# Kernel optimization log

Hardware: AMD Instinct MI355X
Metric: run time of the kernel (lower is better)

Reference implementation:

```python
import jax, jax.numpy as jnp
import numpy as np

N, C, H, W = 64, 128, 32, 32
EPS = 1e-5


def _layernorm_chw(x, w, b):
    # LayerNorm over normalized_shape=(C,H,W): last 3 dims
    mu = jnp.mean(x, axis=(1, 2, 3), keepdims=True)
    var = jnp.var(x, axis=(1, 2, 3), keepdims=True)
    return (x - mu) * jax.lax.rsqrt(var + EPS) * w[None] + b[None]


def _conv1x1(x, w, b):
    # x: [N,C,H,W], w: [Cout,Cin], b: [Cout]
    return jnp.einsum('oc,nchw->nohw', w, x) + b[None, :, None, None]


def setup_inputs() -> dict:
    key = jax.random.key(0)
    ks = jax.random.split(key, 12)
    d = {
        'query': jax.random.normal(ks[0], (N, C, H, W), jnp.float32),
        'key': jax.random.normal(ks[1], (N, C, H, W), jnp.float32),
        'value': jax.random.normal(ks[2], (N, C, H, W), jnp.float32),
        'ln1_w': jnp.ones((C, H, W), jnp.float32),
        'ln1_b': jnp.zeros((C, H, W), jnp.float32),
        'ln2_w': jnp.ones((C, H, W), jnp.float32),
        'ln2_b': jnp.zeros((C, H, W), jnp.float32),
        'ln3_w': jnp.ones((C, H, W), jnp.float32),
        'ln3_b': jnp.zeros((C, H, W), jnp.float32),
        'wq': jax.random.normal(ks[3], (C, C), jnp.float32) / np.sqrt(C),
        'bq': jnp.zeros((C,), jnp.float32),
        'wk': jax.random.normal(ks[4], (C, C), jnp.float32) / np.sqrt(C),
        'bk': jnp.zeros((C,), jnp.float32),
        'wv': jax.random.normal(ks[5], (C, C), jnp.float32) / np.sqrt(C),
        'bv': jnp.zeros((C,), jnp.float32),
    }
    return d


def reference(query, key, value, ln1_w, ln1_b, ln2_w, ln2_b, ln3_w, ln3_b,
              wq, bq, wk, bk, wv, bv):
    qn = _layernorm_chw(query, ln1_w, ln1_b)  # residual uses normalized query
    kn = _layernorm_chw(key, ln2_w, ln2_b)
    vn = _layernorm_chw(value, ln3_w, ln3_b)
    q = _conv1x1(qn, wq, bq).reshape(N, C, H * W)
    k = _conv1x1(kn, wk, bk).reshape(N, C, H * W)
    v = _conv1x1(vn, wv, bv).reshape(N, C, H * W)
    # attention[n,i,j] = sum_c k[n,c,i] q[n,c,j] / sqrt(C); softmax over i (dim=1)
    attn = jnp.einsum('nci,ncj->nij', k, q) / jnp.sqrt(jnp.float32(C))
    attn = jax.nn.softmax(attn, axis=1)
    out = jnp.einsum('nci,nij->ncj', v, attn).reshape(N, C, H, W)
    x = qn + out
    return x.reshape(N, -1)  # flatten(start_dim=1)
```

## Files before the change

kernel.cpp:

```cpp
#include <hip/hip_runtime.h>


#define NS 64
#define CD 128
#define SD 1024
#define MEL (CD*SD)
#define SCALE 0.08838834764831845f

typedef __attribute__((ext_vector_type(4))) float floatx4;
typedef __attribute__((ext_vector_type(8))) short short8;
typedef __attribute__((ext_vector_type(4))) short short4v;

typedef __attribute__((address_space(1))) const void global_cvoid;
typedef __attribute__((address_space(3))) void lds_void;

__device__ __forceinline__ void gl16(const void* g, void* l) {
  __builtin_amdgcn_global_load_lds((global_cvoid*)g, (lds_void*)l, 16, 0, 0);
}
__device__ __forceinline__ unsigned short f2bf(float f) {
  union { float f; unsigned int i; } v; v.f = f;
  unsigned int i = v.i;
  return (unsigned short)((i + 0x7fffu + ((i >> 16) & 1u)) >> 16);
}
__device__ __forceinline__ short8 ld8_bf16(const float* __restrict__ p) {
  floatx4 a = *(const floatx4*)p;
  floatx4 b = *(const floatx4*)(p + 4);
  short8 r;
  r[0] = (short)f2bf(a[0]); r[1] = (short)f2bf(a[1]);
  r[2] = (short)f2bf(a[2]); r[3] = (short)f2bf(a[3]);
  r[4] = (short)f2bf(b[0]); r[5] = (short)f2bf(b[1]);
  r[6] = (short)f2bf(b[2]); r[7] = (short)f2bf(b[3]);
  return r;
}
__device__ __forceinline__ floatx4 mfma16(short8 a, short8 b, floatx4 c) {
  return __builtin_amdgcn_mfma_f32_16x16x32_bf16(a, b, c, 0, 0, 0);
}

__global__ __launch_bounds__(512) void stats_kernel(
    const float* __restrict__ q, const float* __restrict__ k,
    const float* __restrict__ v, float* __restrict__ sums)
{
  int tn = blockIdx.x;
  int part = blockIdx.y;
  int t = tn >> 6;
  const float* x = (t == 0 ? q : (t == 1 ? k : v)) + (size_t)(tn & 63) * MEL
                   + part * (MEL / 2);
  float s1 = 0.f, s2 = 0.f;
  for (int it = 0; it < 32; ++it) {
    floatx4 u = *(const floatx4*)(x + it * 2048 + threadIdx.x * 4);
#pragma unroll
    for (int j = 0; j < 4; ++j) { float f = u[j]; s1 += f; s2 += f * f; }
  }
#pragma unroll
  for (int off = 32; off; off >>= 1) {
    s1 += __shfl_xor(s1, off, 64);
    s2 += __shfl_xor(s2, off, 64);
  }
  __shared__ float r1[8], r2[8];
  int w = threadIdx.x >> 6;
  if ((threadIdx.x & 63) == 0) { r1[w] = s1; r2[w] = s2; }
  __syncthreads();
  if (threadIdx.x == 0) {
    float a = 0.f, b = 0.f;
#pragma unroll
    for (int i = 0; i < 8; ++i) { a += r1[i]; b += r2[i]; }
    sums[part * 192 + tn] = a; sums[384 + part * 192 + tn] = b;
  }
}

__global__ __launch_bounds__(512, 4) void proj_kernel(
  const float* __restrict__ k, const float* __restrict__ v,
  const float* __restrict__ l2w, const float* __restrict__ l2b,
  const float* __restrict__ l3w, const float* __restrict__ l3b,
  const float* __restrict__ wk, const float* __restrict__ bk,
  const float* __restrict__ wv, const float* __restrict__ bv,
  const float* __restrict__ sums,
  unsigned short* __restrict__ kT, unsigned short* __restrict__ vN)
{
  int n  = blockIdx.x, t = blockIdx.y, st = blockIdx.z;
  const float* x  = (t == 0 ? k : v) + (size_t)n * MEL;
  const float* lw = (t == 0 ? l2w : l3w);
  const float* lb = (t == 0 ? l2b : l3b);
  const float* W  = (t == 0 ? wk : wv);
  const float* Bs = (t == 0 ? bk : bv);

  int si = (t + 1) * 64 + n;
  float s1 = sums[si] + sums[192 + si];
  float s2 = sums[384 + si] + sums[576 + si];
  float mu  = s1 * (1.f / MEL);
  float var = s2 * (1.f / MEL) - mu * mu;
  float rs  = rsqrtf(var + 1e-5f);
  float a_ln = rs, b_ln = -mu * rs;

  __shared__ __align__(16) unsigned short Xt[128 * 128];

  int tid = threadIdx.x;
  int cb = tid & 15, sb = (tid >> 4) & 15, half = tid >> 8;
  int s0 = st * 128;

  unsigned int w32[8][2];
#pragma unroll
  for (int pr = 0; pr < 2; ++pr) {
    int c0 = cb * 8 + half * 4 + pr * 2;
    const float* xp0 = x  + (size_t)c0 * SD + s0 + sb * 8;
    const float* wp0 = lw + (size_t)c0 * SD + s0 + sb * 8;
    const float* bp0 = lb + (size_t)c0 * SD + s0 + sb * 8;
    float xv0[8], xv1[8], wv0[8], wv1[8], bv0[8], bv1[8];
    *(floatx4*)xv0 = *(const floatx4*)xp0;       *(floatx4*)(xv0+4) = *(const floatx4*)(xp0+4);
    *(floatx4*)xv1 = *(const floatx4*)(xp0+SD);  *(floatx4*)(xv1+4) = *(const floatx4*)(xp0+SD+4);
    *(floatx4*)wv0 = *(const floatx4*)wp0;       *(floatx4*)(wv0+4) = *(const floatx4*)(wp0+4);
    *(floatx4*)wv1 = *(const floatx4*)(wp0+SD);  *(floatx4*)(wv1+4) = *(const floatx4*)(wp0+SD+4);
    *(floatx4*)bv0 = *(const floatx4*)bp0;       *(floatx4*)(bv0+4) = *(const floatx4*)(bp0+4);
    *(floatx4*)bv1 = *(const floatx4*)(bp0+SD);  *(floatx4*)(bv1+4) = *(const floatx4*)(bp0+SD+4);
#pragma unroll
    for (int js = 0; js < 8; ++js) {
      unsigned int lo = f2bf((xv0[js] * a_ln + b_ln) * wv0[js] + bv0[js]);
      unsigned int hi = f2bf((xv1[js] * a_ln + b_ln) * wv1[js] + bv1[js]);
      w32[js][pr] = lo | (hi << 16);
    }
  }
#pragma unroll
  for (int js = 0; js < 8; ++js) {
    unsigned int* d = (unsigned int*)&Xt[(sb * 8 + js) * 128 + ((cb ^ js) * 8) + half * 4];
    d[0] = w32[js][0]; d[1] = w32[js][1];
  }
  __syncthreads();

  int lane = tid & 63, w = tid >> 6;
  int quad = lane >> 4, l16 = lane & 15;

  short8 Wf[4];
#pragma unroll
  for (int kk = 0; kk < 4; ++kk)
    Wf[kk] = ld8_bf16(W + (w * 16 + l16) * CD + kk * 32 + quad * 8);

  floatx4 acc[8];
  floatx4 zz = {0.f, 0.f, 0.f, 0.f};
#pragma unroll
  for (int sblk = 0; sblk < 8; ++sblk) acc[sblk] = zz;
#pragma unroll
  for (int kk = 0; kk < 4; ++kk)
#pragma unroll
    for (int sblk = 0; sblk < 8; ++sblk) {
      short8 Xf = *(const short8*)&Xt[(sblk * 16 + l16) * 128 +
                                      (((kk * 4 + quad) ^ (l16 & 7)) * 8)];
      acc[sblk] = (t == 0) ? mfma16(Wf[kk], Xf, acc[sblk])
                           : mfma16(Xf, Wf[kk], acc[sblk]);
    }
  __syncthreads();

  if (t == 0) {
    float bsv[4];
#pragma unroll
    for (int r = 0; r < 4; ++r) bsv[r] = Bs[w * 16 + quad * 4 + r];
#pragma unroll
    for (int sblk = 0; sblk < 8; ++sblk) {
      short4v pk;
#pragma unroll
      for (int r = 0; r < 4; ++r) pk[r] = (short)f2bf(acc[sblk][r] + bsv[r]);
      int row = sblk * 16 + l16;
      int cblk = w * 2 + (quad >> 1);
      *(short4v*)&Xt[row * 128 + ((cblk ^ (l16 & 7)) * 8) + (quad & 1) * 4] = pk;
    }
  } else {
    float bsv = Bs[w * 16 + l16];
#pragma unroll
    for (int sblk = 0; sblk < 8; ++sblk) {
      short4v pk;
#pragma unroll
      for (int r = 0; r < 4; ++r) pk[r] = (short)f2bf(acc[sblk][r] + bsv);
      int row = w * 16 + l16;
      int cblk = sblk * 2 + (quad >> 1);
      *(short4v*)&Xt[row * 128 + ((cblk ^ (l16 & 7)) * 8) + (quad & 1) * 4] = pk;
    }
  }
  __syncthreads();

  unsigned short* outp = (t == 0 ? kT : vN);
#pragma unroll
  for (int it = 0; it < 4; ++it) {
    int id = it * 512 + tid;
    int row = id >> 4, ch = id & 15;
    short8 u = *(const short8*)&Xt[row * 128 + ((ch ^ (row & 7)) * 8)];
    size_t g;
    if (t == 0) g = (size_t)n * MEL + (size_t)(s0 + row) * CD + ch * 8;
    else        g = (size_t)n * MEL + (size_t)row * SD + s0 + ch * 8;
    *(short8*)(outp + g) = u;
  }
}

__global__ __launch_bounds__(512, 4) void attn_kernel(
  const float* __restrict__ qraw, const float* __restrict__ l1w,
  const float* __restrict__ l1b, const float* __restrict__ wq,
  const float* __restrict__ bq,
  const unsigned short* __restrict__ kT, const unsigned short* __restrict__ vN,
  const float* __restrict__ sums, float* __restrict__ out)
{
  int n = blockIdx.x, jt = blockIdx.y;
  int j0 = jt * 128;

  __shared__ __align__(16) char smem[33792];
  unsigned short* Xt = (unsigned short*)smem;
  unsigned short* Ks = (unsigned short*)smem;
  unsigned short* Ps = (unsigned short*)smem;
  unsigned short* Vs = (unsigned short*)(smem + 16384);
  float* l_part = (float*)(smem + 32768);

  int tid = threadIdx.x, lane = tid & 63, w = tid >> 6;
  int quad = lane >> 4, l16 = lane & 15;

  float s1 = sums[n] + sums[192 + n];
  float s2 = sums[384 + n] + sums[576 + n];
  float mu  = s1 * (1.f / MEL);
  float var = s2 * (1.f / MEL) - mu * mu;
  float rsd = rsqrtf(var + 1e-5f);
  float a_ln = rsd, b_ln = -mu * rsd;
  const float* qb = qraw + (size_t)n * MEL;

  {
    int cb = tid & 15, sb = (tid >> 4) & 15, half = tid >> 8;
    unsigned int w32[8][2];
#pragma unroll
    for (int pr = 0; pr < 2; ++pr) {
      int c0 = cb * 8 + half * 4 + pr * 2;
      const float* xp0 = qb  + (size_t)c0 * SD + j0 + sb * 8;
      const float* wp0 = l1w + (size_t)c0 * SD + j0 + sb * 8;
      const float* bp0 = l1b + (size_t)c0 * SD + j0 + sb * 8;
      float xv0[8], xv1[8], wv0[8], wv1[8], bv0[8], bv1[8];
      *(floatx4*)xv0 = *(const floatx4*)xp0;       *(floatx4*)(xv0+4) = *(const floatx4*)(xp0+4);
      *(floatx4*)xv1 = *(const floatx4*)(xp0+SD);  *(floatx4*)(xv1+4) = *(const floatx4*)(xp0+SD+4);
      *(floatx4*)wv0 = *(const floatx4*)wp0;       *(floatx4*)(wv0+4) = *(const floatx4*)(wp0+4);
      *(floatx4*)wv1 = *(const floatx4*)(wp0+SD);  *(floatx4*)(wv1+4) = *(const floatx4*)(wp0+SD+4);
      *(floatx4*)bv0 = *(const floatx4*)bp0;       *(floatx4*)(bv0+4) = *(const floatx4*)(bp0+4);
      *(floatx4*)bv1 = *(const floatx4*)(bp0+SD);  *(floatx4*)(bv1+4) = *(const floatx4*)(bp0+SD+4);
#pragma unroll
      for (int js = 0; js < 8; ++js) {
        unsigned int lo = f2bf((xv0[js] * a_ln + b_ln) * wv0[js] + bv0[js]);
        unsigned int hi = f2bf((xv1[js] * a_ln + b_ln) * wv1[js] + bv1[js]);
        w32[js][pr] = lo | (hi << 16);
      }
    }
#pragma unroll
    for (int js = 0; js < 8; ++js) {
      unsigned int* d = (unsigned int*)&Xt[(sb * 8 + js) * 128 + ((cb ^ js) * 8) + half * 4];
      d[0] = w32[js][0]; d[1] = w32[js][1];
    }
  }
  __syncthreads();

  floatx4 zz = {0.f, 0.f, 0.f, 0.f};
  {
    short8 Wf[4];
#pragma unroll
    for (int kk = 0; kk < 4; ++kk)
      Wf[kk] = ld8_bf16(wq + (w * 16 + l16) * CD + kk * 32 + quad * 8);
    floatx4 accq[8];
#pragma unroll
    for (int nb = 0; nb < 8; ++nb) accq[nb] = zz;
#pragma unroll
    for (int kk = 0; kk < 4; ++kk)
#pragma unroll
      for (int nb = 0; nb < 8; ++nb) {
        short8 Bf = *(const short8*)&Xt[(nb * 16 + l16) * 128 +
                                        (((kk * 4 + quad) ^ (l16 & 7)) * 8)];
        accq[nb] = mfma16(Wf[kk], Bf, accq[nb]);
      }
    __syncthreads();
    float bqs[4];
#pragma unroll
    for (int r = 0; r < 4; ++r) bqs[r] = bq[w * 16 + quad * 4 + r];
#pragma unroll
    for (int nb = 0; nb < 8; ++nb) {
      short4v pk;
#pragma unroll
      for (int r = 0; r < 4; ++r) pk[r] = (short)f2bf(accq[nb][r] + bqs[r]);
      int row = nb * 16 + l16;
      int cblk = w * 2 + (quad >> 1);
      *(short4v*)&Xt[row * 128 + ((cblk ^ (l16 & 7)) * 8) + (quad & 1) * 4] = pk;
    }
  }
  __syncthreads();

  short8 Qf[2][4];
#pragma unroll
  for (int ntl = 0; ntl < 2; ++ntl) {
    int row = ((w >> 1) * 2 + ntl) * 16 + l16;
#pragma unroll
    for (int kk = 0; kk < 4; ++kk)
      Qf[ntl][kk] = *(const short8*)&Xt[row * 128 + (((kk * 4 + quad) ^ (l16 & 7)) * 8)];
  }
  __syncthreads();

  floatx4 Oc[2][4];
#pragma unroll
  for (int mi = 0; mi < 2; ++mi)
#pragma unroll
    for (int nb = 0; nb < 4; ++nb) Oc[mi][nb] = zz;
  float lsum[2] = {0.f, 0.f};

  const unsigned short* kbase0 = kT + (size_t)n * MEL;
  const unsigned short* vbase0 = vN + (size_t)n * MEL;

  for (int itile = 0; itile < 16; ++itile) {
    int i0 = itile * 64;
    const unsigned short* kbase = kbase0 + (size_t)i0 * CD;
#pragma unroll
    for (int it = 0; it < 2; ++it) {
      int nch = it * 512 + tid;
      int i = nch >> 4, cc = nch & 15;
      int csrc = (cc & 8) | ((cc & 7) ^ (i & 7));
      gl16(kbase + i * CD + csrc * 8, Ks + nch * 8);
    }
#pragma unroll
    for (int it = 0; it < 2; ++it) {
      int nch = it * 512 + tid;
      int c = nch >> 3, ci = nch & 7;
      int isrc = ci ^ (c & 7);
      gl16(vbase0 + (size_t)c * SD + i0 + isrc * 8, Vs + nch * 8);
    }
    __syncthreads();

    floatx4 Sa[2][2];
#pragma unroll
    for (int a = 0; a < 2; ++a) { Sa[a][0] = zz; Sa[a][1] = zz; }
#pragma unroll
    for (int kk = 0; kk < 4; ++kk) {
      short8 Kf[2];
#pragma unroll
      for (int mtl = 0; mtl < 2; ++mtl) {
        int row = ((w & 1) * 2 + mtl) * 16 + l16;
        Kf[mtl] = *(const short8*)&Ks[row * 128 + (((kk * 4 + quad) ^ (l16 & 7)) * 8)];
      }
#pragma unroll
      for (int mtl = 0; mtl < 2; ++mtl)
#pragma unroll
        for (int ntl = 0; ntl < 2; ++ntl)
          Sa[mtl][ntl] = mfma16(Kf[mtl], Qf[ntl][kk], Sa[mtl][ntl]);
    }
    __syncthreads();

#pragma unroll
    for (int mtl = 0; mtl < 2; ++mtl) {
      int mt = (w & 1) * 2 + mtl;
#pragma unroll
      for (int ntl = 0; ntl < 2; ++ntl) {
        float p0 = __expf(Sa[mtl][ntl][0] * SCALE);
        float p1 = __expf(Sa[mtl][ntl][1] * SCALE);
        float p2 = __expf(Sa[mtl][ntl][2] * SCALE);
        float p3 = __expf(Sa[mtl][ntl][3] * SCALE);
        lsum[ntl] += (p0 + p1) + (p2 + p3);
        short4v pk;
        pk[0] = (short)f2bf(p0); pk[1] = (short)f2bf(p1);
        pk[2] = (short)f2bf(p2); pk[3] = (short)f2bf(p3);
        int jrow = ((w >> 1) * 2 + ntl) * 16 + l16;
        int cis = (mt * 2 + (quad >> 1)) ^ (l16 & 7);
        *(short4v*)&Ps[jrow * 64 + cis * 8 + (quad & 1) * 4] = pk;
      }
    }
    __syncthreads();

#pragma unroll
    for (int kk = 0; kk < 2; ++kk) {
      short8 Vf[2];
#pragma unroll
      for (int mi = 0; mi < 2; ++mi) {
        int c = ((w & 3) * 2 + mi) * 16 + l16;
        Vf[mi] = *(const short8*)&Vs[c * 64 + (((kk * 4 + quad) ^ (l16 & 7)) * 8)];
      }
#pragma unroll
      for (int nb = 0; nb < 4; ++nb) {
        int j = ((w >> 2) * 4 + nb) * 16 + l16;
        short8 Pf = *(const short8*)&Ps[j * 64 + (((kk * 4 + quad) ^ (l16 & 7)) * 8)];
        Oc[0][nb] = mfma16(Vf[0], Pf, Oc[0][nb]);
        Oc[1][nb] = mfma16(Vf[1], Pf, Oc[1][nb]);
      }
    }
    __syncthreads();
  }

#pragma unroll
  for (int ntl = 0; ntl < 2; ++ntl) {
    lsum[ntl] += __shfl_xor(lsum[ntl], 16, 64);
    lsum[ntl] += __shfl_xor(lsum[ntl], 32, 64);
  }
  if (lane < 16) {
#pragma unroll
    for (int ntl = 0; ntl < 2; ++ntl)
      l_part[(w & 1) * 128 + ((w >> 1) * 2 + ntl) * 16 + lane] = lsum[ntl];
  }
  __syncthreads();

  float linv[4];
#pragma unroll
  for (int nb = 0; nb < 4; ++nb) {
    int j = ((w >> 2) * 4 + nb) * 16 + l16;
    linv[nb] = 1.f / (l_part[j] + l_part[128 + j]);
  }
#pragma unroll
  for (int mi = 0; mi < 2; ++mi) {
#pragma unroll
    for (int r = 0; r < 4; ++r) {
      int c = ((w & 3) * 2 + mi) * 16 + quad * 4 + r;
      const float* qp = qb  + (size_t)c * SD + j0;
      const float* wp = l1w + (size_t)c * SD + j0;
      const float* bp = l1b + (size_t)c * SD + j0;
      float* op = out + (size_t)n * MEL + (size_t)c * SD + j0;
#pragma unroll
      for (int nb = 0; nb < 4; ++nb) {
        int j = ((w >> 2) * 4 + nb) * 16 + l16;
        float qn = (qp[j] * a_ln + b_ln) * wp[j] + bp[j];
        op[j] = Oc[mi][nb][r] * linv[nb] + qn;
      }
    }
  }
}

extern "C" void kernel_launch(void* const* d_in, const int* in_sizes, int n_in,
                              void* d_out, int out_size, void* d_ws, size_t ws_size,
                              hipStream_t stream)
{
  const float* q   = (const float*)d_in[0];
  const float* k   = (const float*)d_in[1];
  const float* v   = (const float*)d_in[2];
  const float* l1w = (const float*)d_in[3];
  const float* l1b = (const float*)d_in[4];
  const float* l2w = (const float*)d_in[5];
  const float* l2b = (const float*)d_in[6];
  const float* l3w = (const float*)d_in[7];
  const float* l3b = (const float*)d_in[8];
  const float* wq  = (const float*)d_in[9];
  const float* bq  = (const float*)d_in[10];
  const float* wk  = (const float*)d_in[11];
  const float* bk  = (const float*)d_in[12];
  const float* wv  = (const float*)d_in[13];
  const float* bv  = (const float*)d_in[14];

  char* ws = (char*)d_ws;
  float* sums = (float*)ws;
  unsigned short* kT = (unsigned short*)(ws + 4096);
  unsigned short* vN = kT + (size_t)NS * MEL;

  stats_kernel<<<dim3(192, 2), 512, 0, stream>>>(q, k, v, sums);
  proj_kernel<<<dim3(64, 2, 8), 512, 0, stream>>>(k, v, l2w, l2b, l3w, l3b,
      wk, bk, wv, bv, sums, kT, vN);
  attn_kernel<<<dim3(64, 8), 512, 0, stream>>>(q, l1w, l1b, wq, bq, kT, vN,
      sums, (float*)d_out);
}
```

Measured before the change: 258.4 us.

## Prefetch next K/V tiles during compute and keep normalized query in registers

Measured after the change: 305.9 us. +18.4%, slower.

```diff
diff --git a/kernel.cpp b/kernel.cpp
--- a/kernel.cpp
+++ b/kernel.cpp
@@ -21,6 +21,9 @@
   union { float f; unsigned int i; } v; v.f = f;
   unsigned int i = v.i;
   return (unsigned short)((i + 0x7fffu + ((i >> 16) & 1u)) >> 16);
+}
+__device__ __forceinline__ float bf2f(unsigned short u) {
+  union { unsigned int i; float f; } v; v.i = ((unsigned int)u) << 16; return v.f;
 }
 __device__ __forceinline__ short8 ld8_bf16(const float* __restrict__ p) {
   floatx4 a = *(const floatx4*)p;
@@ -199,12 +202,12 @@
   int n = blockIdx.x, jt = blockIdx.y;
   int j0 = jt * 128;
 
-  __shared__ __align__(16) char smem[33792];
+  __shared__ __align__(16) char smem[50176];
   unsigned short* Xt = (unsigned short*)smem;
   unsigned short* Ks = (unsigned short*)smem;
-  unsigned short* Ps = (unsigned short*)smem;
   unsigned short* Vs = (unsigned short*)(smem + 16384);
-  float* l_part = (float*)(smem + 32768);
+  unsigned short* Ps = (unsigned short*)(smem + 32768);
+  float* l_part = (float*)(smem + 49152);
 
   int tid = threadIdx.x, lane = tid & 63, w = tid >> 6;
   int quad = lane >> 4, l16 = lane & 15;
@@ -217,33 +220,31 @@
   float a_ln = rsd, b_ln = -mu * rsd;
   const float* qb = qraw + (size_t)n * MEL;
 
-  {
-    int cb = tid & 15, sb = (tid >> 4) & 15, half = tid >> 8;
-    unsigned int w32[8][2];
-#pragma unroll
-    for (int pr = 0; pr < 2; ++pr) {
-      int c0 = cb * 8 + half * 4 + pr * 2;
-      const float* xp0 = qb  + (size_t)c0 * SD + j0 + sb * 8;
-      const float* wp0 = l1w + (size_t)c0 * SD + j0 + sb * 8;
-      const float* bp0 = l1b + (size_t)c0 * SD + j0 + sb * 8;
-      float xv0[8], xv1[8], wv0[8], wv1[8], bv0[8], bv1[8];
-      *(floatx4*)xv0 = *(const floatx4*)xp0;       *(floatx4*)(xv0+4) = *(const floatx4*)(xp0+4);
-      *(floatx4*)xv1 = *(const floatx4*)(xp0+SD);  *(floatx4*)(xv1+4) = *(const floatx4*)(xp0+SD+4);
-      *(floatx4*)wv0 = *(const floatx4*)wp0;       *(floatx4*)(wv0+4) = *(const floatx4*)(wp0+4);
-      *(floatx4*)wv1 = *(const floatx4*)(wp0+SD);  *(floatx4*)(wv1+4) = *(const floatx4*)(wp0+SD+4);
-      *(floatx4*)bv0 = *(const floatx4*)bp0;       *(floatx4*)(bv0+4) = *(const floatx4*)(bp0+4);
-      *(floatx4*)bv1 = *(const floatx4*)(bp0+SD);  *(floatx4*)(bv1+4) = *(const floatx4*)(bp0+SD+4);
-#pragma unroll
-      for (int js = 0; js < 8; ++js) {
-        unsigned int lo = f2bf((xv0[js] * a_ln + b_ln) * wv0[js] + bv0[js]);
-        unsigned int hi = f2bf((xv1[js] * a_ln + b_ln) * wv1[js] + bv1[js]);
-        w32[js][pr] = lo | (hi << 16);
-      }
-    }
-#pragma unroll
-    for (int js = 0; js < 8; ++js) {
-      unsigned int* d = (unsigned int*)&Xt[(sb * 8 + js) * 128 + ((cb ^ js) * 8) + half * 4];
-      d[0] = w32[js][0]; d[1] = w32[js][1];
+  short4v qn_pk[2][4];
+#pragma unroll
+  for (int mi = 0; mi < 2; ++mi) {
+    float qnf[4][4];
+#pragma unroll
+    for (int r = 0; r < 4; ++r) {
+      int c = ((w & 3) * 2 + mi) * 16 + quad * 4 + r;
+      const float* qp = qb  + (size_t)c * SD + j0;
+      const float* wp = l1w + (size_t)c * SD + j0;
+      const float* bp = l1b + (size_t)c * SD + j0;
+#pragma unroll
+      for (int nb = 0; nb < 4; ++nb) {
+        int j = ((w >> 2) * 4 + nb) * 16 + l16;
+        qnf[r][nb] = (qp[j] * a_ln + b_ln) * wp[j] + bp[j];
+      }
+    }
+#pragma unroll
+    for (int nb = 0; nb < 4; ++nb) {
+      short4v pk;
+#pragma unroll
+      for (int r = 0; r < 4; ++r) pk[r] = (short)f2bf(qnf[r][nb]);
+      qn_pk[mi][nb] = pk;
+      int jl = ((w >> 2) * 4 + nb) * 16 + l16;
+      int cblk = ((w & 3) * 2 + mi) * 2 + (quad >> 1);
+      *(short4v*)&Xt[jl * 128 + ((cblk ^ (l16 & 7)) * 8) + (quad & 1) * 4] = pk;
     }
   }
   __syncthreads();
@@ -301,25 +302,30 @@
   const unsigned short* kbase0 = kT + (size_t)n * MEL;
   const unsigned short* vbase0 = vN + (size_t)n * MEL;
 
-  for (int itile = 0; itile < 16; ++itile) {
-    int i0 = itile * 64;
-    const unsigned short* kbase = kbase0 + (size_t)i0 * CD;
-#pragma unroll
-    for (int it = 0; it < 2; ++it) {
-      int nch = it * 512 + tid;
-      int i = nch >> 4, cc = nch & 15;
-      int csrc = (cc & 8) | ((cc & 7) ^ (i & 7));
-      gl16(kbase + i * CD + csrc * 8, Ks + nch * 8);
-    }
-#pragma unroll
-    for (int it = 0; it < 2; ++it) {
-      int nch = it * 512 + tid;
-      int c = nch >> 3, ci = nch & 7;
-      int isrc = ci ^ (c & 7);
-      gl16(vbase0 + (size_t)c * SD + i0 + isrc * 8, Vs + nch * 8);
-    }
-    __syncthreads();
-
+#define STAGE_K(T) {                                                        \
+    const unsigned short* kb = kbase0 + (size_t)(T) * 64 * CD;              \
+    _Pragma("unroll")                                                       \
+    for (int it = 0; it < 2; ++it) {                                        \
+      int nch = it * 512 + tid;                                             \
+      int i = nch >> 4, cc = nch & 15;                                      \
+      int csrc = (cc & 8) | ((cc & 7) ^ (i & 7));                           \
+      gl16(kb + i * CD + csrc * 8, Ks + nch * 8);                           \
+    } }
+#define STAGE_V(T) {                                                        \
+    int i0 = (T) * 64;                                                      \
+    _Pragma("unroll")                                                       \
+    for (int it = 0; it < 2; ++it) {                                        \
+      int nch = it * 512 + tid;                                             \
+      int c = nch >> 3, ci = nch & 7;                                       \
+      int isrc = ci ^ (c & 7);                                              \
+      gl16(vbase0 + (size_t)c * SD + i0 + isrc * 8, Vs + nch * 8);          \
+    } }
+
+  STAGE_K(0);
+  STAGE_V(0);
+  __syncthreads();
+
+  for (int t = 0; t < 16; ++t) {
     floatx4 Sa[2][2];
 #pragma unroll
     for (int a = 0; a < 2; ++a) { Sa[a][0] = zz; Sa[a][1] = zz; }
@@ -337,7 +343,6 @@
         for (int ntl = 0; ntl < 2; ++ntl)
           Sa[mtl][ntl] = mfma16(Kf[mtl], Qf[ntl][kk], Sa[mtl][ntl]);
     }
-    __syncthreads();
 
 #pragma unroll
     for (int mtl = 0; mtl < 2; ++mtl) {
@@ -359,6 +364,8 @@
     }
     __syncthreads();
 
+    if (t < 15) STAGE_K(t + 1);
+
 #pragma unroll
     for (int kk = 0; kk < 2; ++kk) {
       short8 Vf[2];
@@ -376,6 +383,8 @@
       }
     }
     __syncthreads();
+
+    if (t < 15) STAGE_V(t + 1);
   }
 
 #pragma unroll
@@ -401,18 +410,17 @@
 #pragma unroll
     for (int r = 0; r < 4; ++r) {
       int c = ((w & 3) * 2 + mi) * 16 + quad * 4 + r;
-      const float* qp = qb  + (size_t)c * SD + j0;
-      const float* wp = l1w + (size_t)c * SD + j0;
-      const float* bp = l1b + (size_t)c * SD + j0;
       float* op = out + (size_t)n * MEL + (size_t)c * SD + j0;
 #pragma unroll
       for (int nb = 0; nb < 4; ++nb) {
         int j = ((w >> 2) * 4 + nb) * 16 + l16;
-        float qn = (qp[j] * a_ln + b_ln) * wp[j] + bp[j];
+        float qn = bf2f((unsigned short)qn_pk[mi][nb][r]);
         op[j] = Oc[mi][nb][r] * linv[nb] + qn;
       }
     }
   }
+#undef STAGE_K
+#undef STAGE_V
 }
 
 extern "C" void kernel_launch(void* const* d_in, const int* in_sizes, int n_in,
```
